# Kernel optimization log

Hardware: AMD Instinct MI355X
Metric: run time of the kernel (lower is better)

## Reference

```python
import jax, jax.numpy as jnp
import numpy as np

B, C, T, H, Wd = 8, 256, 16, 28, 28

def setup_inputs() -> dict:
    key = jax.random.key(0)
    k1, k2 = jax.random.split(key)
    in_data = jax.random.normal(k1, (B, C, T, H, Wd), dtype=jnp.float32)
    # conv_whh weight [C, C, 1, 1, 1] squeezed to [C_out, C_in]; scaled like kaiming init
    W = jax.random.normal(k2, (C, C), dtype=jnp.float32) * (1.0 / jnp.sqrt(jnp.float32(C)))
    return {"in_data": in_data, "W": W}

def reference(in_data, W):
    # h_0 = x_0; h_t = (W @ h_{t-1} + x_t) / 2, out = stack over t
    x0 = in_data[:, :, 0]                      # [B, C, H, W]
    xs = jnp.moveaxis(in_data[:, :, 1:], 2, 0) # [T-1, B, C, H, W]

    def step(h, x_t):
        h_new = (jnp.einsum('oc,bchw->bohw', W, h) + x_t) * 0.5
        return h_new, h_new

    _, outs = jax.lax.scan(step, x0, xs)       # [T-1, B, C, H, W]
    out = jnp.concatenate([x0[None], outs], axis=0)  # [T, B, C, H, W]
    return jnp.moveaxis(out, 0, 2)             # [B, C, T, H, W]
```

## Files before the change

### kernel.cpp

```cpp
#include <hip/hip_runtime.h>


typedef __attribute__((ext_vector_type(8))) short bf16x8;
typedef __attribute__((ext_vector_type(4))) float f32x4;
typedef __attribute__((ext_vector_type(4))) short short4v;

#define NTILES 49
#define LDSK   264

__device__ __forceinline__ short f2bf(float f) {
    union { float f; unsigned u; } v; v.f = f;
    unsigned r = v.u + 0x7FFFu + ((v.u >> 16) & 1u);
    return (short)(r >> 16);
}

__global__ __launch_bounds__(256, 2)
void rcu_kernel(const float* __restrict__ in, const float* __restrict__ Wm,
                float* __restrict__ out) {
    __shared__ short hbuf[2][16][LDSK];

    const int tid  = threadIdx.x;
    const int wave = tid >> 6;
    const int lane = tid & 63;
    const int l15  = lane & 15;
    const int quad = lane >> 4;

    const int b  = blockIdx.x / NTILES;
    const int s0 = (blockIdx.x % NTILES) * 16;

    bf16x8 a_frag[4][8];
#pragma unroll
    for (int mt = 0; mt < 4; ++mt) {
        const int m = wave * 64 + mt * 16 + l15;
        const float* wrow = Wm + m * 256 + quad * 8;
#pragma unroll
        for (int ks = 0; ks < 8; ++ks) {
            float4 f0 = *(const float4*)(wrow + ks * 32);
            float4 f1 = *(const float4*)(wrow + ks * 32 + 4);
            bf16x8 a;
            a[0] = f2bf(f0.x); a[1] = f2bf(f0.y); a[2] = f2bf(f0.z); a[3] = f2bf(f0.w);
            a[4] = f2bf(f1.x); a[5] = f2bf(f1.y); a[6] = f2bf(f1.z); a[7] = f2bf(f1.w);
            a_frag[mt][ks] = a;
        }
    }

    const size_t base = (size_t)b * 256 * 16 * 784 + s0;
    const float* xin  = in  + base;
    float*       xout = out + base;

    {
        const int sg = tid & 15;
        const int cg = tid >> 4;
#pragma unroll
        for (int i = 0; i < 16; ++i) {
            const int c = cg * 16 + i;
            const size_t off = (size_t)c * 16 * 784 + sg;
            const float v = xin[off];
            xout[off] = v;
            hbuf[0][sg][c] = f2bf(v);
        }
    }
    __syncthreads();

    int cur = 0;
    for (int t = 1; t < 16; ++t) {
        bf16x8 bfrag[8];
        const short* hp = &hbuf[cur][l15][quad * 8];
#pragma unroll
        for (int ks = 0; ks < 8; ++ks)
            bfrag[ks] = *(const bf16x8*)(hp + ks * 32);

        const int nxt = cur ^ 1;
#pragma unroll
        for (int mt = 0; mt < 4; ++mt) {
            f32x4 acc = {0.f, 0.f, 0.f, 0.f};
#pragma unroll
            for (int ks = 0; ks < 8; ++ks)
                acc = __builtin_amdgcn_mfma_f32_16x16x32_bf16(a_frag[mt][ks], bfrag[ks], acc, 0, 0, 0);

            const int c0 = wave * 64 + mt * 16 + quad * 4;
            short4v hbf;
#pragma unroll
            for (int r = 0; r < 4; ++r) {
                const size_t off = ((size_t)(c0 + r) * 16 + t) * 784 + l15;
                const float v = 0.5f * (acc[r] + xin[off]);
                xout[off] = v;
                hbf[r] = f2bf(v);
            }
            *(short4v*)&hbuf[nxt][l15][c0] = hbf;
        }
        __syncthreads();
        cur = nxt;
    }
}

extern "C" void kernel_launch(void* const* d_in, const int* in_sizes, int n_in,
                              void* d_out, int out_size, void* d_ws, size_t ws_size,
                              hipStream_t stream) {
    const float* in  = (const float*)d_in[0];
    const float* Wm  = (const float*)d_in[1];
    float*       out = (float*)d_out;
    hipLaunchKernelGGL(rcu_kernel, dim3(8 * NTILES), dim3(256), 0, stream, in, Wm, out);
}
```

Baseline: 232.0 us.

## Prefetch next timestep input into LDS with async global-to-LDS loads

Each timestep's input slice is now streamed into a double-buffered LDS array with global_load_lds, one step ahead of the recurrence. The epilogue then reads x_t from LDS instead of issuing dependent global loads after the MFMA chain. This hides global memory latency behind the matrix multiply of the previous step. The cost is about 32 KB of extra LDS per block, which may limit occupancy, and correctness depends on the barrier waiting for the async loads to land.

```diff
diff --git a/kernel.cpp b/kernel.cpp
--- a/kernel.cpp
+++ b/kernel.cpp
@@ -7,6 +7,11 @@
 
 #define NTILES 49
 #define LDSK   264
+
+#define ASYNC16(gsrc, ldst)                                                    \
+    __builtin_amdgcn_global_load_lds(                                          \
+        (const __attribute__((address_space(1))) void*)(gsrc),                 \
+        (__attribute__((address_space(3))) void*)(ldst), 16, 0, 0)
 
 __device__ __forceinline__ short f2bf(float f) {
     union { float f; unsigned u; } v; v.f = f;
@@ -18,6 +23,7 @@
 void rcu_kernel(const float* __restrict__ in, const float* __restrict__ Wm,
                 float* __restrict__ out) {
     __shared__ short hbuf[2][16][LDSK];
+    __shared__ float xlds[2][256][16];
 
     const int tid  = threadIdx.x;
     const int wave = tid >> 6;
@@ -27,6 +33,19 @@
 
     const int b  = blockIdx.x / NTILES;
     const int s0 = (blockIdx.x % NTILES) * 16;
+
+    const size_t base = (size_t)b * 256 * 16 * 784 + s0;
+    const float* xin  = in  + base;
+    float*       xout = out + base;
+
+    const int cidx = lane >> 2;
+    const int sq   = (lane & 3) * 4;
+
+#pragma unroll
+    for (int i = 0; i < 4; ++i) {
+        const int cbi = (wave * 4 + i) * 16;
+        ASYNC16(xin + (size_t)(cbi + cidx) * 12544 + sq, &xlds[0][cbi][0]);
+    }
 
     bf16x8 a_frag[4][8];
 #pragma unroll
@@ -44,9 +63,13 @@
         }
     }
 
-    const size_t base = (size_t)b * 256 * 16 * 784 + s0;
-    const float* xin  = in  + base;
-    float*       xout = out + base;
+#pragma unroll
+    for (int i = 0; i < 4; ++i) {
+        const int cbi = (wave * 4 + i) * 16;
+        ASYNC16(xin + (size_t)(cbi + cidx) * 12544 + 784 + sq, &xlds[1][cbi][0]);
+    }
+
+    __syncthreads();
 
     {
         const int sg = tid & 15;
@@ -54,9 +77,8 @@
 #pragma unroll
         for (int i = 0; i < 16; ++i) {
             const int c = cg * 16 + i;
-            const size_t off = (size_t)c * 16 * 784 + sg;
-            const float v = xin[off];
-            xout[off] = v;
+            const float v = xlds[0][c][sg];
+            xout[(size_t)c * 12544 + sg] = v;
             hbuf[0][sg][c] = f2bf(v);
         }
     }
@@ -64,6 +86,17 @@
 
     int cur = 0;
     for (int t = 1; t < 16; ++t) {
+        const int xb = t & 1;
+
+        if (t < 15) {
+#pragma unroll
+            for (int i = 0; i < 4; ++i) {
+                const int cbi = (wave * 4 + i) * 16;
+                ASYNC16(xin + (size_t)(cbi + cidx) * 12544 + (size_t)(t + 1) * 784 + sq,
+                        &xlds[xb ^ 1][cbi][0]);
+            }
+        }
+
         bf16x8 bfrag[8];
         const short* hp = &hbuf[cur][l15][quad * 8];
 #pragma unroll
@@ -82,9 +115,9 @@
             short4v hbf;
 #pragma unroll
             for (int r = 0; r < 4; ++r) {
-                const size_t off = ((size_t)(c0 + r) * 16 + t) * 784 + l15;
-                const float v = 0.5f * (acc[r] + xin[off]);
-                xout[off] = v;
+                const float xv = xlds[xb][c0 + r][l15];
+                const float v  = 0.5f * (acc[r] + xv);
+                xout[((size_t)(c0 + r) * 16 + t) * 784 + l15] = v;
                 hbf[r] = f2bf(v);
             }
             *(short4v*)&hbuf[nxt][l15][c0] = hbf;
```

Result: no change. 228.7 us (-1.4%).

## Prefetch next timestep inputs into registers and use LDS-only barriers

Applied to the files above, without the earlier changes.

Loads the x_{t+1} inputs into a double-buffered register array while step t runs, so global load latency is hidden behind the MFMA chain instead of sitting on the serial recurrence path. Replaces __syncthreads with a barrier that waits only on LDS counters, so outstanding global loads and stores no longer stall the barrier. The time loop is fully unrolled and all four MFMA accumulations are issued before the epilogue. This raises register pressure under launch_bounds(256,2), which could cause spills or lower occupancy.

```diff
diff --git a/kernel.cpp b/kernel.cpp
--- a/kernel.cpp
+++ b/kernel.cpp
@@ -7,6 +7,13 @@
 
 #define NTILES 49
 #define LDSK   264
+
+#define LDS_BARRIER()                                                          \
+    do {                                                                       \
+        asm volatile("s_waitcnt lgkmcnt(0)" ::: "memory");                     \
+        __builtin_amdgcn_s_barrier();                                          \
+        __builtin_amdgcn_sched_barrier(0);                                     \
+    } while (0)
 
 __device__ __forceinline__ short f2bf(float f) {
     union { float f; unsigned u; } v; v.f = f;
@@ -28,6 +35,10 @@
     const int b  = blockIdx.x / NTILES;
     const int s0 = (blockIdx.x % NTILES) * 16;
 
+    const size_t base = (size_t)b * 256 * 16 * 784 + s0;
+    const float* xin  = in  + base;
+    float*       xout = out + base;
+
     bf16x8 a_frag[4][8];
 #pragma unroll
     for (int mt = 0; mt < 4; ++mt) {
@@ -44,52 +55,77 @@
         }
     }
 
-    const size_t base = (size_t)b * 256 * 16 * 784 + s0;
-    const float* xin  = in  + base;
-    float*       xout = out + base;
-
     {
         const int sg = tid & 15;
         const int cg = tid >> 4;
 #pragma unroll
         for (int i = 0; i < 16; ++i) {
             const int c = cg * 16 + i;
-            const size_t off = (size_t)c * 16 * 784 + sg;
+            const size_t off = (size_t)c * 12544 + sg;
             const float v = xin[off];
             xout[off] = v;
             hbuf[0][sg][c] = f2bf(v);
         }
     }
-    __syncthreads();
+
+    float xr[2][16];
+
+#pragma unroll
+    for (int mt = 0; mt < 4; ++mt)
+#pragma unroll
+        for (int r = 0; r < 4; ++r) {
+            const int c = wave * 64 + mt * 16 + quad * 4 + r;
+            xr[1][mt * 4 + r] = xin[((size_t)c * 16 + 1) * 784 + l15];
+        }
+
+    LDS_BARRIER();
 
     int cur = 0;
+#pragma unroll
     for (int t = 1; t < 16; ++t) {
+        const int xb = t & 1;
+
+        if (t < 15) {
+#pragma unroll
+            for (int mt = 0; mt < 4; ++mt)
+#pragma unroll
+                for (int r = 0; r < 4; ++r) {
+                    const int c = wave * 64 + mt * 16 + quad * 4 + r;
+                    xr[xb ^ 1][mt * 4 + r] =
+                        xin[((size_t)c * 16 + t + 1) * 784 + l15];
+                }
+        }
+
         bf16x8 bfrag[8];
         const short* hp = &hbuf[cur][l15][quad * 8];
 #pragma unroll
         for (int ks = 0; ks < 8; ++ks)
             bfrag[ks] = *(const bf16x8*)(hp + ks * 32);
 
+        f32x4 acc[4];
+#pragma unroll
+        for (int mt = 0; mt < 4; ++mt) {
+            acc[mt] = (f32x4){0.f, 0.f, 0.f, 0.f};
+#pragma unroll
+            for (int ks = 0; ks < 8; ++ks)
+                acc[mt] = __builtin_amdgcn_mfma_f32_16x16x32_bf16(
+                    a_frag[mt][ks], bfrag[ks], acc[mt], 0, 0, 0);
+        }
+
         const int nxt = cur ^ 1;
 #pragma unroll
         for (int mt = 0; mt < 4; ++mt) {
-            f32x4 acc = {0.f, 0.f, 0.f, 0.f};
-#pragma unroll
-            for (int ks = 0; ks < 8; ++ks)
-                acc = __builtin_amdgcn_mfma_f32_16x16x32_bf16(a_frag[mt][ks], bfrag[ks], acc, 0, 0, 0);
-
             const int c0 = wave * 64 + mt * 16 + quad * 4;
             short4v hbf;
 #pragma unroll
             for (int r = 0; r < 4; ++r) {
-                const size_t off = ((size_t)(c0 + r) * 16 + t) * 784 + l15;
-                const float v = 0.5f * (acc[r] + xin[off]);
-                xout[off] = v;
+                const float v = 0.5f * (acc[mt][r] + xr[xb][mt * 4 + r]);
+                xout[((size_t)(c0 + r) * 16 + t) * 784 + l15] = v;
                 hbf[r] = f2bf(v);
             }
             *(short4v*)&hbuf[nxt][l15][c0] = hbf;
         }
-        __syncthreads();
+        LDS_BARRIER();
         cur = nxt;
     }
 }
```

Result: no change. 229.5 us (-1.1%).
